# Kernel optimization log

Measured on AMD Instinct MI355X. Metric: run time of the kernel, lower is better.

## Reference

```python
import jax, jax.numpy as jnp
import numpy as np

N = 50000      # nodes
E = 640000     # edges
F_IN = 128     # input features
H = 128        # hidden = 2**7
C = 40         # classes


def setup_inputs() -> dict:
    key = jax.random.key(0)
    ks = jax.random.split(key, 10)
    x = jax.random.normal(ks[0], (N, F_IN), dtype=jnp.float32)
    edge_index = jax.random.randint(ks[1], (2, E), 0, N, dtype=jnp.int32)
    edge_weight = jax.random.uniform(ks[2], (E,), dtype=jnp.float32)
    def glorot(k, fan_in, fan_out):
        s = (6.0 / (fan_in + fan_out)) ** 0.5
        return jax.random.uniform(k, (fan_in, fan_out), jnp.float32, -s, s)
    return {
        "x": x,
        "edge_index": edge_index,
        "edge_weight": edge_weight,
        "W1": glorot(ks[3], F_IN, H), "b1": jnp.zeros((H,), jnp.float32),
        "W2": glorot(ks[4], H, H),    "b2": jnp.zeros((H,), jnp.float32),
        "W3": glorot(ks[5], H, C),    "b3": jnp.zeros((C,), jnp.float32),
    }


def gcn_conv(x, W, b, src, dst, ew, n):
    """PyG GCNConv: add self-loops, symmetric deg normalization, gather-scatter-add."""
    loop = jnp.arange(n, dtype=src.dtype)
    src_sl = jnp.concatenate([src, loop])
    dst_sl = jnp.concatenate([dst, loop])
    w_sl = jnp.concatenate([ew, jnp.ones((n,), ew.dtype)])
    deg = jax.ops.segment_sum(w_sl, dst_sl, num_segments=n)         # [N]
    dinv = jnp.where(deg > 0, jax.lax.rsqrt(deg), 0.0)
    norm = dinv[src_sl] * w_sl * dinv[dst_sl]                        # [E+N]
    h = x @ W                                                        # [N, out]
    msg = h[src_sl] * norm[:, None]                                  # gather + scale
    out = jax.ops.segment_sum(msg, dst_sl, num_segments=n)          # scatter-add
    return out + b


def reference(x, edge_index, edge_weight, W1, b1, W2, b2, W3, b3):
    # eval-mode forward: dropout and dropedge are identity (training=False)
    src, dst = edge_index[0], edge_index[1]
    n = x.shape[0]
    h = jax.nn.relu(gcn_conv(x, W1, b1, src, dst, edge_weight, n))
    h = jax.nn.relu(gcn_conv(h, W2, b2, src, dst, edge_weight, n))
    return gcn_conv(h, W3, b3, src, dst, edge_weight, n)
```

## Files before the change

### kernel.cpp

```cpp
#include <hip/hip_runtime.h>
#include <hip/hip_fp16.h>

constexpr int N_NODES = 50000;
constexpr int N_EDGES = 640000;

constexpr int NBLK  = 256;
constexpr int EPB   = N_EDGES / NBLK;
constexpr int NBUCK = (N_NODES + 255) / 256;
constexpr int GB128 = (N_NODES + 31) / 32;


template<typename TIN, bool FUSE_HIST>
__global__ __launch_bounds__(256) void gemm128_k(const TIN* __restrict__ X,
        const float* __restrict__ W, __half* __restrict__ H,
        const int* __restrict__ dst, int* __restrict__ gh) {
    if constexpr (FUSE_HIST) {
        if (blockIdx.x < NBLK) {
            __shared__ int lh[256];
            int t = threadIdx.x, b = blockIdx.x;
            lh[t] = 0;
            __syncthreads();
            int e0 = b * EPB;
            for (int j = t; j < EPB; j += 256)
                atomicAdd(&lh[dst[e0 + j] >> 8], 1);
            __syncthreads();
            if (t < NBUCK) gh[b * NBUCK + t] = lh[t];
            return;
        }
    }
    int bid = FUSE_HIST ? (int)blockIdx.x - NBLK : (int)blockIdx.x;

    constexpr int RB = 32;
    __shared__ float4 xs4[RB * 32];
    int tid = threadIdx.x;
    int row0 = bid * RB;

    int rows_in = N_NODES - row0; if (rows_in > RB) rows_in = RB;
    int limit4 = rows_in * 32;
    for (int idx = tid; idx < RB * 32; idx += 256) {
        float4 v = {0.f, 0.f, 0.f, 0.f};
        if (idx < limit4) {
            if constexpr (sizeof(TIN) == 4) {
                v = ((const float4*)(X + (size_t)row0 * 128))[idx];
            } else {
                int2 raw = ((const int2*)(X + (size_t)row0 * 128))[idx];
                __half2 a = *(__half2*)&raw.x;
                __half2 bq = *(__half2*)&raw.y;
                float2 fa = __half22float2(a), fb = __half22float2(bq);
                v = make_float4(fa.x, fa.y, fb.x, fb.y);
            }
        }
        xs4[idx] = v;
    }
    __syncthreads();

    int cg = tid & 31;
    int rg = tid >> 5;
    const float4* Wg = (const float4*)W;

    float4 acc[4];
    #pragma unroll
    for (int r = 0; r < 4; r++) acc[r] = make_float4(0.f, 0.f, 0.f, 0.f);

    #pragma unroll 2
    for (int kc = 0; kc < 32; kc++) {
        float4 w0 = Wg[(4 * kc + 0) * 32 + cg];
        float4 w1 = Wg[(4 * kc + 1) * 32 + cg];
        float4 w2 = Wg[(4 * kc + 2) * 32 + cg];
        float4 w3 = Wg[(4 * kc + 3) * 32 + cg];
        #pragma unroll
        for (int r = 0; r < 4; r++) {
            float4 a = xs4[(rg * 4 + r) * 32 + kc];
            acc[r].x = fmaf(a.x, w0.x, acc[r].x);
            acc[r].y = fmaf(a.x, w0.y, acc[r].y);
            acc[r].z = fmaf(a.x, w0.z, acc[r].z);
            acc[r].w = fmaf(a.x, w0.w, acc[r].w);
            acc[r].x = fmaf(a.y, w1.x, acc[r].x);
            acc[r].y = fmaf(a.y, w1.y, acc[r].y);
            acc[r].z = fmaf(a.y, w1.z, acc[r].z);
            acc[r].w = fmaf(a.y, w1.w, acc[r].w);
            acc[r].x = fmaf(a.z, w2.x, acc[r].x);
            acc[r].y = fmaf(a.z, w2.y, acc[r].y);
            acc[r].z = fmaf(a.z, w2.z, acc[r].z);
            acc[r].w = fmaf(a.z, w2.w, acc[r].w);
            acc[r].x = fmaf(a.w, w3.x, acc[r].x);
            acc[r].y = fmaf(a.w, w3.y, acc[r].y);
            acc[r].z = fmaf(a.w, w3.z, acc[r].z);
            acc[r].w = fmaf(a.w, w3.w, acc[r].w);
        }
    }

    #pragma unroll
    for (int r = 0; r < 4; r++) {
        int row = row0 + rg * 4 + r;
        if (row < N_NODES) {
            __half2 h0 = __float22half2_rn(make_float2(acc[r].x, acc[r].y));
            __half2 h1 = __float22half2_rn(make_float2(acc[r].z, acc[r].w));
            int2 o; o.x = *(int*)&h0; o.y = *(int*)&h1;
            *(int2*)&H[(size_t)row * 128 + cg * 4] = o;
        }
    }
}


__global__ __launch_bounds__(256) void gemm40_k(const __half* __restrict__ X,
        const float* __restrict__ W, __half* __restrict__ Y) {
    constexpr int F_OUT = 40, F_PAD = 64;
    constexpr int RB  = 32;
    constexpr int CG  = F_PAD / 4;
    constexpr int RG  = 256 / CG;
    constexpr int RPT = RB / RG;
    __shared__ float xs[RB * 128];
    __shared__ float ws[128 * F_PAD];
    int tid = threadIdx.x;
    int row0 = blockIdx.x * RB;

    for (int idx = tid; idx < 128 * F_PAD; idx += 256) {
        int k = idx / F_PAD, c = idx - k * F_PAD;
        ws[idx] = (c < F_OUT) ? W[k * F_OUT + c] : 0.f;
    }
    int rows_in = N_NODES - row0; if (rows_in > RB) rows_in = RB;
    int limit4 = rows_in * 32;
    float4* xs4 = (float4*)xs;
    for (int idx = tid; idx < RB * 32; idx += 256) {
        float4 v = {0.f, 0.f, 0.f, 0.f};
        if (idx < limit4) {
            int2 raw = ((const int2*)(X + (size_t)row0 * 128))[idx];
            __half2 a = *(__half2*)&raw.x;
            __half2 bq = *(__half2*)&raw.y;
            float2 fa = __half22float2(a), fb = __half22float2(bq);
            v = make_float4(fa.x, fa.y, fb.x, fb.y);
        }
        xs4[idx] = v;
    }
    __syncthreads();

    int cg = tid % CG, rg = tid / CG;
    float acc[RPT][4];
    #pragma unroll
    for (int r = 0; r < RPT; r++) { acc[r][0] = acc[r][1] = acc[r][2] = acc[r][3] = 0.f; }

    #pragma unroll 4
    for (int k = 0; k < 128; k++) {
        float4 wv = *(const float4*)&ws[k * F_PAD + cg * 4];
        #pragma unroll
        for (int r = 0; r < RPT; r++) {
            float a = xs[(rg * RPT + r) * 128 + k];
            acc[r][0] = fmaf(a, wv.x, acc[r][0]);
            acc[r][1] = fmaf(a, wv.y, acc[r][1]);
            acc[r][2] = fmaf(a, wv.z, acc[r][2]);
            acc[r][3] = fmaf(a, wv.w, acc[r][3]);
        }
    }

    #pragma unroll
    for (int r = 0; r < RPT; r++) {
        int row = row0 + rg * RPT + r;
        int cb = cg * 4;
        if (row < N_NODES && cb < F_OUT) {
            __half2 h0 = __float22half2_rn(make_float2(acc[r][0], acc[r][1]));
            __half2 h1 = __float22half2_rn(make_float2(acc[r][2], acc[r][3]));
            int2 o; o.x = *(int*)&h0; o.y = *(int*)&h1;
            *(int2*)&Y[(size_t)row * F_OUT + cb] = o;
        }
    }
}


__global__ __launch_bounds__(256) void scan1_k(int* __restrict__ gh, int* __restrict__ total) {
    __shared__ int s[256];
    int t = threadIdx.x, b = blockIdx.x;
    int v = gh[t * NBUCK + b];
    s[t] = v;
    __syncthreads();
    int x = v;
    for (int off = 1; off < 256; off <<= 1) {
        int u = (t >= off) ? s[t - off] : 0;
        __syncthreads();
        x += u; s[t] = x;
        __syncthreads();
    }
    gh[t * NBUCK + b] = x - v;
    if (t == 255) total[b] = x;
}

__global__ __launch_bounds__(256) void scan2_k(const int* __restrict__ total,
                                               int* __restrict__ bbase) {
    __shared__ int s[256];
    int t = threadIdx.x;
    int v = (t < NBUCK) ? total[t] : 0;
    s[t] = v;
    __syncthreads();
    int x = v;
    for (int off = 1; off < 256; off <<= 1) {
        int u = (t >= off) ? s[t - off] : 0;
        __syncthreads();
        x += u; s[t] = x;
        __syncthreads();
    }
    if (t <= NBUCK) bbase[t] = x - v;
}


__global__ __launch_bounds__(256) void bucket_k(const int* __restrict__ src,
        const int* __restrict__ dst, const float* __restrict__ ew,
        const int* __restrict__ gh, const int* __restrict__ bbase,
        int2* __restrict__ bkt) {
    __shared__ int cur[256];
    int t = threadIdx.x, b = blockIdx.x;
    if (t < NBUCK) cur[t] = bbase[t] + gh[b * NBUCK + t];
    __syncthreads();
    int e0 = b * EPB;
    for (int j = t; j < EPB; j += 256) {
        int d = dst[e0 + j];
        int pos = atomicAdd(&cur[d >> 8], 1);
        bkt[pos] = make_int2(src[e0 + j] | (d << 16), __float_as_int(ew[e0 + j]));
    }
}


__global__ __launch_bounds__(256) void final_k(const int2* __restrict__ bkt,
        const int* __restrict__ bbase, int2* __restrict__ ev,
        int* __restrict__ rowptr, float* __restrict__ dinv) {
    __shared__ int   cnt[256];
    __shared__ float wsum[256];
    __shared__ int   s[256];
    int t = threadIdx.x, b = blockIdx.x;
    int base = bbase[b], cntb = bbase[b + 1] - base;
    cnt[t] = 0; wsum[t] = 0.f;
    __syncthreads();
    for (int j = t; j < cntb; j += 256) {
        int2 r = bkt[base + j];
        int bin = (r.x >> 16) & 255;
        atomicAdd(&cnt[bin], 1);
        atomicAdd(&wsum[bin], __int_as_float(r.y));
    }
    __syncthreads();
    int v = cnt[t];
    s[t] = v;
    __syncthreads();
    int x = v;
    for (int off = 1; off < 256; off <<= 1) {
        int u = (t >= off) ? s[t - off] : 0;
        __syncthreads();
        x += u; s[t] = x;
        __syncthreads();
    }
    int off_t = x - v;
    int nd = b * 256 + t;
    if (nd < N_NODES) {
        rowptr[nd] = base + off_t;
        dinv[nd] = rsqrtf(1.0f + wsum[t]);
    }
    if (b == 0 && t == 0) rowptr[N_NODES] = N_EDGES;
    s[t] = off_t;
    __syncthreads();
    for (int j = t; j < cntb; j += 256) {
        int2 r = bkt[base + j];
        int bin = (r.x >> 16) & 255;
        int p = atomicAdd(&s[bin], 1);
        ev[base + p] = make_int2(r.x & 0xFFFF, r.y);
    }
}


__global__ __launch_bounds__(256) void agg128_k(const __half* __restrict__ H,
        const int2* __restrict__ ev, const int* __restrict__ rowptr,
        const float* __restrict__ dinv, const float* __restrict__ bias,
        __half* __restrict__ out) {
    int lane = threadIdx.x & 63;
    int node = __builtin_amdgcn_readfirstlane(blockIdx.x * 4 + (threadIdx.x >> 6));
    if (node >= N_NODES) return;
    const __half2* __restrict__ H2 = (const __half2*)H;
    float di = dinv[node];
    float2 hs = __half22float2(H2[(size_t)node * 64 + lane]);
    float ax = di * hs.x, ay = di * hs.y;
    int e0 = rowptr[node], e1 = rowptr[node + 1];
    int e = e0;
    for (; e + 4 <= e1; e += 4) {
        int2 p0 = ev[e + 0];
        int2 p1 = ev[e + 1];
        int2 p2 = ev[e + 2];
        int2 p3 = ev[e + 3];
        float d0 = dinv[p0.x], d1 = dinv[p1.x], d2 = dinv[p2.x], d3 = dinv[p3.x];
        float2 g0 = __half22float2(H2[(size_t)p0.x * 64 + lane]);
        float2 g1 = __half22float2(H2[(size_t)p1.x * 64 + lane]);
        float2 g2 = __half22float2(H2[(size_t)p2.x * 64 + lane]);
        float2 g3 = __half22float2(H2[(size_t)p3.x * 64 + lane]);
        float v0 = __int_as_float(p0.y) * d0;
        float v1 = __int_as_float(p1.y) * d1;
        float v2 = __int_as_float(p2.y) * d2;
        float v3 = __int_as_float(p3.y) * d3;
        ax = fmaf(v0, g0.x, ax); ay = fmaf(v0, g0.y, ay);
        ax = fmaf(v1, g1.x, ax); ay = fmaf(v1, g1.y, ay);
        ax = fmaf(v2, g2.x, ax); ay = fmaf(v2, g2.y, ay);
        ax = fmaf(v3, g3.x, ax); ay = fmaf(v3, g3.y, ay);
    }
    for (; e < e1; e++) {
        int2 p = ev[e];
        float v = __int_as_float(p.y) * dinv[p.x];
        float2 g = __half22float2(H2[(size_t)p.x * 64 + lane]);
        ax = fmaf(v, g.x, ax);
        ay = fmaf(v, g.y, ay);
    }
    float2 b = *(const float2*)&bias[2 * lane];
    ax = fmaxf(fmaf(ax, di, b.x), 0.f);
    ay = fmaxf(fmaf(ay, di, b.y), 0.f);
    ((__half2*)out)[(size_t)node * 64 + lane] = __float22half2_rn(make_float2(ax, ay));
}


__global__ __launch_bounds__(256) void agg40_k(const __half* __restrict__ Y,
        const int2* __restrict__ ev, const int* __restrict__ rowptr,
        const float* __restrict__ dinv, const float* __restrict__ bias,
        float* __restrict__ out) {
    int lane = threadIdx.x & 63;
    int node = __builtin_amdgcn_readfirstlane(blockIdx.x * 4 + (threadIdx.x >> 6));
    if (node >= N_NODES) return;
    const __half2* __restrict__ Y2 = (const __half2*)Y;
    int f = (lane < 20) ? lane : 0;
    float di = dinv[node];
    float2 ys = __half22float2(Y2[(size_t)node * 20 + f]);
    float ax = di * ys.x, ay = di * ys.y;
    int e0 = rowptr[node], e1 = rowptr[node + 1];
    int e = e0;
    for (; e + 4 <= e1; e += 4) {
        int2 p0 = ev[e + 0];
        int2 p1 = ev[e + 1];
        int2 p2 = ev[e + 2];
        int2 p3 = ev[e + 3];
        float d0 = dinv[p0.x], d1 = dinv[p1.x], d2 = dinv[p2.x], d3 = dinv[p3.x];
        float2 g0 = __half22float2(Y2[(size_t)p0.x * 20 + f]);
        float2 g1 = __half22float2(Y2[(size_t)p1.x * 20 + f]);
        float2 g2 = __half22float2(Y2[(size_t)p2.x * 20 + f]);
        float2 g3 = __half22float2(Y2[(size_t)p3.x * 20 + f]);
        float v0 = __int_as_float(p0.y) * d0;
        float v1 = __int_as_float(p1.y) * d1;
        float v2 = __int_as_float(p2.y) * d2;
        float v3 = __int_as_float(p3.y) * d3;
        ax = fmaf(v0, g0.x, ax); ay = fmaf(v0, g0.y, ay);
        ax = fmaf(v1, g1.x, ax); ay = fmaf(v1, g1.y, ay);
        ax = fmaf(v2, g2.x, ax); ay = fmaf(v2, g2.y, ay);
        ax = fmaf(v3, g3.x, ax); ay = fmaf(v3, g3.y, ay);
    }
    for (; e < e1; e++) {
        int2 p = ev[e];
        float v = __int_as_float(p.y) * dinv[p.x];
        float2 g = __half22float2(Y2[(size_t)p.x * 20 + f]);
        ax = fmaf(v, g.x, ax);
        ay = fmaf(v, g.y, ay);
    }
    if (lane < 20) {
        float2 b = *(const float2*)&bias[2 * lane];
        float2 o;
        o.x = fmaf(ax, di, b.x);
        o.y = fmaf(ay, di, b.y);
        *(float2*)&out[(size_t)node * 40 + 2 * lane] = o;
    }
}


extern "C" void kernel_launch(void* const* d_in, const int* in_sizes, int n_in,
                              void* d_out, int out_size, void* d_ws, size_t ws_size,
                              hipStream_t stream) {
    const float* x  = (const float*)d_in[0];
    const int*   ei = (const int*)d_in[1];
    const int*   src = ei;
    const int*   dst = ei + N_EDGES;
    const float* ew = (const float*)d_in[2];
    const float* W1 = (const float*)d_in[3];
    const float* b1 = (const float*)d_in[4];
    const float* W2 = (const float*)d_in[5];
    const float* b2 = (const float*)d_in[6];
    const float* W3 = (const float*)d_in[7];
    const float* b3 = (const float*)d_in[8];
    float* out = (float*)d_out;

    char* w = (char*)d_ws;
    auto alloc = [&](size_t bytes) {
        char* p = w;
        w += (bytes + 255) & ~(size_t)255;
        return p;
    };
    float*  dinv   = (float*) alloc((size_t)N_NODES * 4);
    int*    rowptr = (int*)   alloc((size_t)(N_NODES + 1) * 4);
    int*    gh     = (int*)   alloc((size_t)NBLK * NBUCK * 4);
    int*    total  = (int*)   alloc((size_t)NBUCK * 4);
    int*    bbase  = (int*)   alloc((size_t)(NBUCK + 1) * 4);
    int2*   bkt    = (int2*)  alloc((size_t)N_EDGES * 8);
    int2*   ev     = (int2*)  alloc((size_t)N_EDGES * 8);
    __half* hbuf   = (__half*)alloc((size_t)N_NODES * 128 * 2);
    __half* abuf   = (__half*)alloc((size_t)N_NODES * 128 * 2);
    __half* ybuf   = (__half*)alloc((size_t)N_NODES * 40 * 2);

    constexpr int GA = (N_NODES + 3) / 4;

    gemm128_k<float, true><<<NBLK + GB128, 256, 0, stream>>>(x, W1, hbuf, dst, gh);
    scan1_k<<<NBUCK, 256, 0, stream>>>(gh, total);
    scan2_k<<<1, 256, 0, stream>>>(total, bbase);
    bucket_k<<<NBLK, 256, 0, stream>>>(src, dst, ew, gh, bbase, bkt);
    final_k<<<NBUCK, 256, 0, stream>>>(bkt, bbase, ev, rowptr, dinv);

    agg128_k<<<GA, 256, 0, stream>>>(hbuf, ev, rowptr, dinv, b1, abuf);
    gemm128_k<__half, false><<<GB128, 256, 0, stream>>>(abuf, W2, hbuf, nullptr, nullptr);
    agg128_k<<<GA, 256, 0, stream>>>(hbuf, ev, rowptr, dinv, b2, abuf);
    gemm40_k<<<GB128, 256, 0, stream>>>(abuf, W3, ybuf);
    agg40_k<<<GA, 256, 0, stream>>>(ybuf, ev, rowptr, dinv, b3, out);
}
```

Before: 293.1 us.

## Replace scalar FMA GEMMs with fp16 MFMA kernels using pre-transposed weights

```diff
diff --git a/kernel.cpp b/kernel.cpp
--- a/kernel.cpp
+++ b/kernel.cpp
@@ -7,12 +7,33 @@
 constexpr int NBLK  = 256;
 constexpr int EPB   = N_EDGES / NBLK;
 constexpr int NBUCK = (N_NODES + 255) / 256;
-constexpr int GB128 = (N_NODES + 31) / 32;
-
-
-template<typename TIN, bool FUSE_HIST>
-__global__ __launch_bounds__(256) void gemm128_k(const TIN* __restrict__ X,
-        const float* __restrict__ W, __half* __restrict__ H,
+constexpr int GBM   = (N_NODES + 63) / 64;
+
+typedef _Float16 half8  __attribute__((ext_vector_type(8)));
+typedef _Float16 half4v __attribute__((ext_vector_type(4)));
+typedef float    floatx4 __attribute__((ext_vector_type(4)));
+
+
+__global__ void wconv_k(const float* __restrict__ W1, const float* __restrict__ W2,
+                        const float* __restrict__ W3, _Float16* __restrict__ Wt1,
+                        _Float16* __restrict__ Wt2, _Float16* __restrict__ Wt3) {
+    int i = blockIdx.x * 256 + threadIdx.x;
+    if (i < 16384) {
+        int n = i >> 7, k = i & 127;
+        Wt1[n * 128 + k] = (_Float16)W1[k * 128 + n];
+    } else if (i < 32768) {
+        int j = i - 16384; int n = j >> 7, k = j & 127;
+        Wt2[n * 128 + k] = (_Float16)W2[k * 128 + n];
+    } else if (i < 32768 + 6144) {
+        int j = i - 32768; int n = j >> 7, k = j & 127;
+        Wt3[n * 128 + k] = (_Float16)((n < 40) ? W3[k * 40 + n] : 0.f);
+    }
+}
+
+
+template<typename TIN, int F_OUT, int NT, bool FUSE_HIST>
+__global__ __launch_bounds__(256) void gemm_mfma_k(const TIN* __restrict__ X,
+        const _Float16* __restrict__ Wt, __half* __restrict__ H,
         const int* __restrict__ dst, int* __restrict__ gh) {
     if constexpr (FUSE_HIST) {
         if (blockIdx.x < NBLK) {
@@ -30,138 +51,81 @@
     }
     int bid = FUSE_HIST ? (int)blockIdx.x - NBLK : (int)blockIdx.x;
 
-    constexpr int RB = 32;
-    __shared__ float4 xs4[RB * 32];
+    __shared__ _Float16 Xs[64 * 136];
     int tid = threadIdx.x;
-    int row0 = bid * RB;
-
-    int rows_in = N_NODES - row0; if (rows_in > RB) rows_in = RB;
-    int limit4 = rows_in * 32;
-    for (int idx = tid; idx < RB * 32; idx += 256) {
-        float4 v = {0.f, 0.f, 0.f, 0.f};
-        if (idx < limit4) {
-            if constexpr (sizeof(TIN) == 4) {
-                v = ((const float4*)(X + (size_t)row0 * 128))[idx];
-            } else {
-                int2 raw = ((const int2*)(X + (size_t)row0 * 128))[idx];
-                __half2 a = *(__half2*)&raw.x;
-                __half2 bq = *(__half2*)&raw.y;
-                float2 fa = __half22float2(a), fb = __half22float2(bq);
-                v = make_float4(fa.x, fa.y, fb.x, fb.y);
-            }
-        }
-        xs4[idx] = v;
-    }
-    __syncthreads();
-
-    int cg = tid & 31;
-    int rg = tid >> 5;
-    const float4* Wg = (const float4*)W;
-
-    float4 acc[4];
+    int row0 = bid * 64;
+
+    if constexpr (sizeof(TIN) == 4) {
+        for (int idx = tid; idx < 2048; idx += 256) {
+            int r = idx >> 5, c4 = idx & 31;
+            float4 v = {0.f, 0.f, 0.f, 0.f};
+            if (row0 + r < N_NODES)
+                v = *(const float4*)((const float*)X + (size_t)(row0 + r) * 128 + c4 * 4);
+            half4v h;
+            h[0] = (_Float16)v.x; h[1] = (_Float16)v.y;
+            h[2] = (_Float16)v.z; h[3] = (_Float16)v.w;
+            *(half4v*)&Xs[r * 136 + c4 * 4] = h;
+        }
+    } else {
+        for (int idx = tid; idx < 1024; idx += 256) {
+            int r = idx >> 4, c8 = idx & 15;
+            int4 v = {0, 0, 0, 0};
+            if (row0 + r < N_NODES)
+                v = *(const int4*)((const __half*)X + (size_t)(row0 + r) * 128 + c8 * 8);
+            *(int4*)&Xs[r * 136 + c8 * 8] = v;
+        }
+    }
+    __syncthreads();
+
+    int lane = tid & 63;
+    int wv   = tid >> 6;
+    int m    = lane & 15;
+    int q    = lane >> 4;
+
+    half8 af[4];
     #pragma unroll
-    for (int r = 0; r < 4; r++) acc[r] = make_float4(0.f, 0.f, 0.f, 0.f);
-
-    #pragma unroll 2
-    for (int kc = 0; kc < 32; kc++) {
-        float4 w0 = Wg[(4 * kc + 0) * 32 + cg];
-        float4 w1 = Wg[(4 * kc + 1) * 32 + cg];
-        float4 w2 = Wg[(4 * kc + 2) * 32 + cg];
-        float4 w3 = Wg[(4 * kc + 3) * 32 + cg];
+    for (int kt = 0; kt < 4; kt++)
+        af[kt] = *(const half8*)&Xs[(wv * 16 + m) * 136 + kt * 32 + q * 8];
+
+    floatx4 acc[NT];
+    #pragma unroll
+    for (int nt = 0; nt < NT; nt++) { acc[nt][0] = 0.f; acc[nt][1] = 0.f; acc[nt][2] = 0.f; acc[nt][3] = 0.f; }
+
+    #pragma unroll
+    for (int nt = 0; nt < NT; nt++) {
+        const _Float16* wp = Wt + (size_t)(nt * 16 + m) * 128 + q * 8;
+        half8 b0 = *(const half8*)(wp);
+        half8 b1 = *(const half8*)(wp + 32);
+        half8 b2 = *(const half8*)(wp + 64);
+        half8 b3 = *(const half8*)(wp + 96);
+        acc[nt] = __builtin_amdgcn_mfma_f32_16x16x32_f16(af[0], b0, acc[nt], 0, 0, 0);
+        acc[nt] = __builtin_amdgcn_mfma_f32_16x16x32_f16(af[1], b1, acc[nt], 0, 0, 0);
+        acc[nt] = __builtin_amdgcn_mfma_f32_16x16x32_f16(af[2], b2, acc[nt], 0, 0, 0);
+        acc[nt] = __builtin_amdgcn_mfma_f32_16x16x32_f16(af[3], b3, acc[nt], 0, 0, 0);
+    }
+
+    #pragma unroll
+    for (int nt = 0; nt < NT; nt++) {
         #pragma unroll
-        for (int r = 0; r < 4; r++) {
-            float4 a = xs4[(rg * 4 + r) * 32 + kc];
-            acc[r].x = fmaf(a.x, w0.x, acc[r].x);
-            acc[r].y = fmaf(a.x, w0.y, acc[r].y);
-            acc[r].z = fmaf(a.x, w0.z, acc[r].z);
-            acc[r].w = fmaf(a.x, w0.w, acc[r].w);
-            acc[r].x = fmaf(a.y, w1.x, acc[r].x);
-            acc[r].y = fmaf(a.y, w1.y, acc[r].y);
-            acc[r].z = fmaf(a.y, w1.z, acc[r].z);
-            acc[r].w = fmaf(a.y, w1.w, acc[r].w);
-            acc[r].x = fmaf(a.z, w2.x, acc[r].x);
-            acc[r].y = fmaf(a.z, w2.y, acc[r].y);
-            acc[r].z = fmaf(a.z, w2.z, acc[r].z);
-            acc[r].w = fmaf(a.z, w2.w, acc[r].w);
-            acc[r].x = fmaf(a.w, w3.x, acc[r].x);
-            acc[r].y = fmaf(a.w, w3.y, acc[r].y);
-            acc[r].z = fmaf(a.w, w3.z, acc[r].z);
-            acc[r].w = fmaf(a.w, w3.w, acc[r].w);
-        }
-    }
-
-    #pragma unroll
-    for (int r = 0; r < 4; r++) {
-        int row = row0 + rg * 4 + r;
-        if (row < N_NODES) {
-            __half2 h0 = __float22half2_rn(make_float2(acc[r].x, acc[r].y));
-            __half2 h1 = __float22half2_rn(make_float2(acc[r].z, acc[r].w));
-            int2 o; o.x = *(int*)&h0; o.y = *(int*)&h1;
-            *(int2*)&H[(size_t)row * 128 + cg * 4] = o;
-        }
-    }
-}
-
-
-__global__ __launch_bounds__(256) void gemm40_k(const __half* __restrict__ X,
-        const float* __restrict__ W, __half* __restrict__ Y) {
-    constexpr int F_OUT = 40, F_PAD = 64;
-    constexpr int RB  = 32;
-    constexpr int CG  = F_PAD / 4;
-    constexpr int RG  = 256 / CG;
-    constexpr int RPT = RB / RG;
-    __shared__ float xs[RB * 128];
-    __shared__ float ws[128 * F_PAD];
-    int tid = threadIdx.x;
-    int row0 = blockIdx.x * RB;
-
-    for (int idx = tid; idx < 128 * F_PAD; idx += 256) {
-        int k = idx / F_PAD, c = idx - k * F_PAD;
-        ws[idx] = (c < F_OUT) ? W[k * F_OUT + c] : 0.f;
-    }
-    int rows_in = N_NODES - row0; if (rows_in > RB) rows_in = RB;
-    int limit4 = rows_in * 32;
-    float4* xs4 = (float4*)xs;
-    for (int idx = tid; idx < RB * 32; idx += 256) {
-        float4 v = {0.f, 0.f, 0.f, 0.f};
-        if (idx < limit4) {
-            int2 raw = ((const int2*)(X + (size_t)row0 * 128))[idx];
-            __half2 a = *(__half2*)&raw.x;
-            __half2 bq = *(__half2*)&raw.y;
-            float2 fa = __half22float2(a), fb = __half22float2(bq);
-            v = make_float4(fa.x, fa.y, fb.x, fb.y);
-        }
-        xs4[idx] = v;
-    }
-    __syncthreads();
-
-    int cg = tid % CG, rg = tid / CG;
-    float acc[RPT][4];
-    #pragma unroll
-    for (int r = 0; r < RPT; r++) { acc[r][0] = acc[r][1] = acc[r][2] = acc[r][3] = 0.f; }
-
-    #pragma unroll 4
-    for (int k = 0; k < 128; k++) {
-        float4 wv = *(const float4*)&ws[k * F_PAD + cg * 4];
-        #pragma unroll
-        for (int r = 0; r < RPT; r++) {
-            float a = xs[(rg * RPT + r) * 128 + k];
-            acc[r][0] = fmaf(a, wv.x, acc[r][0]);
-            acc[r][1] = fmaf(a, wv.y, acc[r][1]);
-            acc[r][2] = fmaf(a, wv.z, acc[r][2]);
-            acc[r][3] = fmaf(a, wv.w, acc[r][3]);
-        }
-    }
-
-    #pragma unroll
-    for (int r = 0; r < RPT; r++) {
-        int row = row0 + rg * RPT + r;
-        int cb = cg * 4;
-        if (row < N_NODES && cb < F_OUT) {
-            __half2 h0 = __float22half2_rn(make_float2(acc[r][0], acc[r][1]));
-            __half2 h1 = __float22half2_rn(make_float2(acc[r][2], acc[r][3]));
-            int2 o; o.x = *(int*)&h0; o.y = *(int*)&h1;
-            *(int2*)&Y[(size_t)row * F_OUT + cb] = o;
+        for (int r = 0; r < 4; r++)
+            Xs[(wv * 16 + q * 4 + r) * 136 + nt * 16 + m] = (_Float16)acc[nt][r];
+    }
+
+    if constexpr (F_OUT == 128) {
+        for (int g = lane; g < 256; g += 64) {
+            int r = g >> 4, c8 = g & 15;
+            int row = row0 + wv * 16 + r;
+            if (row < N_NODES)
+                *(int4*)((__half*)H + (size_t)row * 128 + c8 * 8) =
+                    *(const int4*)&Xs[(wv * 16 + r) * 136 + c8 * 8];
+        }
+    } else {
+        for (int g = lane; g < 80; g += 64) {
+            int r = g / 5, seg = g - r * 5;
+            int row = row0 + wv * 16 + r;
+            if (row < N_NODES)
+                *(int4*)((__half*)H + (size_t)row * 40 + seg * 8) =
+                    *(const int4*)&Xs[(wv * 16 + r) * 136 + seg * 8];
         }
     }
 }
@@ -382,28 +346,32 @@
         w += (bytes + 255) & ~(size_t)255;
         return p;
     };
-    float*  dinv   = (float*) alloc((size_t)N_NODES * 4);
-    int*    rowptr = (int*)   alloc((size_t)(N_NODES + 1) * 4);
-    int*    gh     = (int*)   alloc((size_t)NBLK * NBUCK * 4);
-    int*    total  = (int*)   alloc((size_t)NBUCK * 4);
-    int*    bbase  = (int*)   alloc((size_t)(NBUCK + 1) * 4);
-    int2*   bkt    = (int2*)  alloc((size_t)N_EDGES * 8);
-    int2*   ev     = (int2*)  alloc((size_t)N_EDGES * 8);
-    __half* hbuf   = (__half*)alloc((size_t)N_NODES * 128 * 2);
-    __half* abuf   = (__half*)alloc((size_t)N_NODES * 128 * 2);
-    __half* ybuf   = (__half*)alloc((size_t)N_NODES * 40 * 2);
+    float*     dinv   = (float*)    alloc((size_t)N_NODES * 4);
+    int*       rowptr = (int*)      alloc((size_t)(N_NODES + 1) * 4);
+    int*       gh     = (int*)      alloc((size_t)NBLK * NBUCK * 4);
+    int*       total  = (int*)      alloc((size_t)NBUCK * 4);
+    int*       bbase  = (int*)      alloc((size_t)(NBUCK + 1) * 4);
+    int2*      bkt    = (int2*)     alloc((size_t)N_EDGES * 8);
+    int2*      ev     = (int2*)     alloc((size_t)N_EDGES * 8);
+    __half*    hbuf   = (__half*)   alloc((size_t)N_NODES * 128 * 2);
+    __half*    abuf   = (__half*)   alloc((size_t)N_NODES * 128 * 2);
+    __half*    ybuf   = (__half*)   alloc((size_t)N_NODES * 40 * 2);
+    _Float16*  Wt1    = (_Float16*) alloc((size_t)128 * 128 * 2);
+    _Float16*  Wt2    = (_Float16*) alloc((size_t)128 * 128 * 2);
+    _Float16*  Wt3    = (_Float16*) alloc((size_t)48 * 128 * 2);
 
     constexpr int GA = (N_NODES + 3) / 4;
 
-    gemm128_k<float, true><<<NBLK + GB128, 256, 0, stream>>>(x, W1, hbuf, dst, gh);
+    wconv_k<<<152, 256, 0, stream>>>(W1, W2, W3, Wt1, Wt2, Wt3);
+    gemm_mfma_k<float, 128, 8, true><<<NBLK + GBM, 256, 0, stream>>>(x, Wt1, hbuf, dst, gh);
     scan1_k<<<NBUCK, 256, 0, stream>>>(gh, total);
     scan2_k<<<1, 256, 0, stream>>>(total, bbase);
     bucket_k<<<NBLK, 256, 0, stream>>>(src, dst, ew, gh, bbase, bkt);
     final_k<<<NBUCK, 256, 0, stream>>>(bkt, bbase, ev, rowptr, dinv);
 
     agg128_k<<<GA, 256, 0, stream>>>(hbuf, ev, rowptr, dinv, b1, abuf);
-    gemm128_k<__half, false><<<GB128, 256, 0, stream>>>(abuf, W2, hbuf, nullptr, nullptr);
+    gemm_mfma_k<__half, 128, 8, false><<<GBM, 256, 0, stream>>>(abuf, Wt2, hbuf, nullptr, nullptr);
     agg128_k<<<GA, 256, 0, stream>>>(hbuf, ev, rowptr, dinv, b2, abuf);
-    gemm40_k<<<GB128, 256, 0, stream>>>(abuf, W3, ybuf);
+    gemm_mfma_k<__half, 40, 3, false><<<GBM, 256, 0, stream>>>(abuf, Wt3, ybuf, nullptr, nullptr);
     agg40_k<<<GA, 256, 0, stream>>>(ybuf, ev, rowptr, dinv, b3, out);
 }
```

Result: faster. 251.9 us (-14.1%).
